# Kernel tuning notes

Hardware: AMD Instinct MI355X
Metric: run time of the kernel (lower is better)

The kernel has to match this reference:

```python
import jax, jax.numpy as jnp
import numpy as np

B, D, H, DH, NQ, NK = 64, 768, 8, 128, 256, 256


def _ln(x, g, b, eps=1e-5):
    m = x.mean(-1, keepdims=True)
    v = ((x - m) ** 2).mean(-1, keepdims=True)
    return (x - m) / jnp.sqrt(v + eps) * g + b


def setup_inputs() -> dict:
    key = jax.random.key(0)
    ks = jax.random.split(key, 16)
    w = lambda k, s: jax.random.normal(k, s, jnp.float32) * 0.02
    return {
        'emb_cause': jax.random.normal(ks[0], (B, D), jnp.float32),
        'emb_action': jax.random.normal(ks[1], (B, D), jnp.float32),
        'tok_cause': jax.random.normal(ks[2], (B, NK, D), jnp.float32),
        'tok_effect': jax.random.normal(ks[3], (B, NQ, D), jnp.float32),
        'fuse_ln_g': jnp.ones(2 * D), 'fuse_ln_b': jnp.zeros(2 * D),
        'fuse_w1': w(ks[4], (2 * D, D)), 'fuse_b1': jnp.zeros(D),
        'fuse_w2': w(ks[5], (D, D)), 'fuse_b2': jnp.zeros(D),
        'delta_ln_g': jnp.ones(D), 'delta_ln_b': jnp.zeros(D),
        'delta_w': w(ks[6], (D, D)), 'delta_b': jnp.zeros(D),
        'qg_w': w(ks[7], (D, H * DH)), 'qg_b': jnp.zeros(H * DH),
        'kg_w': w(ks[8], (D, H * DH)), 'kg_b': jnp.zeros(H * DH),
        'eff_ln_g': jnp.ones(D), 'eff_ln_b': jnp.zeros(D),
        'eff_w1': w(ks[9], (D, D)), 'eff_b1': jnp.zeros(D),
        'eff_w2': w(ks[10], (D, D)), 'eff_b2': jnp.zeros(D),
        'u_w': w(ks[11], (D, H * DH)),
        'v_w': w(ks[12], (D, H * DH)),
        'logit_scale': jnp.zeros(()),
    }


def reference(emb_cause, emb_action, tok_cause, tok_effect,
              fuse_ln_g, fuse_ln_b, fuse_w1, fuse_b1, fuse_w2, fuse_b2,
              delta_ln_g, delta_ln_b, delta_w, delta_b,
              qg_w, qg_b, kg_w, kg_b,
              eff_ln_g, eff_ln_b, eff_w1, eff_b1, eff_w2, eff_b2,
              u_w, v_w, logit_scale):
    # fuse: LN -> Linear -> GELU(exact) -> Linear (dropout = identity, eval)
    ctx_in = jnp.concatenate([emb_cause, emb_action], axis=-1)  # (B, 2D)
    h = jax.nn.gelu(_ln(ctx_in, fuse_ln_g, fuse_ln_b) @ fuse_w1 + fuse_b1, approximate=False)
    ctx = h @ fuse_w2 + fuse_b2  # (B, D)

    delta_e = _ln(ctx, delta_ln_g, delta_ln_b) @ delta_w + delta_b  # (B, D)
    pooled_effect = tok_effect.mean(axis=1)  # (B, D)
    e_shifted = pooled_effect + delta_e

    eh = jax.nn.gelu(_ln(ctx, eff_ln_g, eff_ln_b) @ eff_w1 + eff_b1, approximate=False)
    effect_pred = eh @ eff_w2 + eff_b2  # (B, D)

    q_gate = 1.0 + jnp.tanh(jax.nn.silu(ctx @ qg_w + qg_b)).reshape(B, H, DH)
    k_gate = 1.0 + jnp.tanh(jax.nn.silu(ctx @ kg_w + kg_b)).reshape(B, H, DH)

    # logit bias: torch code materializes (B,H,Nq,Nk,Dh); equivalent math is a
    # per-head inner product u.v (independent of q) broadcast over Nq.
    u = (e_shifted @ u_w).reshape(B, H, DH)            # (B, H, Dh)
    v = (tok_cause @ v_w).reshape(B, NK, H, DH)        # (B, Nk, H, Dh)
    bias = jnp.einsum('bhd,bkhd->bhk', u, v) / np.float32(np.sqrt(DH))
    logit_bias = jnp.exp(logit_scale) * jnp.broadcast_to(bias[:, :, None, :], (B, H, NQ, NK))

    return (q_gate, k_gate, e_shifted, delta_e, logit_bias, effect_pred)
```

## Files before the change

kernel.cpp:

```cpp
#include <hip/hip_runtime.h>
#include <math.h>

#define TPB 256

typedef float vf4 __attribute__((ext_vector_type(4)));

__device__ __forceinline__ float gelu_f(float x) {
    return 0.5f * x * (1.0f + erff(x * 0.70710678118654752f));
}
__device__ __forceinline__ float gate_f(float x) {
    float si = x / (1.0f + expf(-x));
    return 1.0f + tanhf(si);
}

template <class XL>
__device__ __forceinline__ void gemm_tile(XL xload, const float* __restrict__ W, int Wld, int cb,
                                          int k0, int kslice, float* part, int totN, int gcol, int s,
                                          float* __restrict__ xs, float* __restrict__ wt)
{
    const int t = threadIdx.x;
    const int tr4 = (t >> 4) << 2;
    const int tc4 = (t & 15) << 2;
    const int a  = t >> 5, kk = t & 31;
    const int wk = t >> 6, wc = t & 63;
    float xv[8], wv[8];
#pragma unroll
    for (int j = 0; j < 8; ++j) {
        xv[j] = xload(a + 8 * j, k0 + kk);
        wv[j] = W[(size_t)(k0 + wk + 4 * j) * Wld + cb + wc];
    }
    float acc[4][4] = {{0.f,0.f,0.f,0.f},{0.f,0.f,0.f,0.f},{0.f,0.f,0.f,0.f},{0.f,0.f,0.f,0.f}};
    for (int kc = 0; kc < kslice; kc += 32) {
#pragma unroll
        for (int j = 0; j < 8; ++j) {
            xs[kk * 68 + a + 8 * j] = xv[j];
            wt[(wk + 4 * j) * 68 + wc] = wv[j];
        }
        __syncthreads();
        int kn = kc + 32;
        if (kn < kslice) {
#pragma unroll
            for (int j = 0; j < 8; ++j) {
                xv[j] = xload(a + 8 * j, k0 + kn + kk);
                wv[j] = W[(size_t)(k0 + kn + wk + 4 * j) * Wld + cb + wc];
            }
        }
#pragma unroll
        for (int k = 0; k < 32; ++k) {
            float4 xq = *(const float4*)&xs[k * 68 + tr4];
            float4 wq = *(const float4*)&wt[k * 68 + tc4];
            acc[0][0] += xq.x * wq.x; acc[0][1] += xq.x * wq.y; acc[0][2] += xq.x * wq.z; acc[0][3] += xq.x * wq.w;
            acc[1][0] += xq.y * wq.x; acc[1][1] += xq.y * wq.y; acc[1][2] += xq.y * wq.z; acc[1][3] += xq.y * wq.w;
            acc[2][0] += xq.z * wq.x; acc[2][1] += xq.z * wq.y; acc[2][2] += xq.z * wq.z; acc[2][3] += xq.z * wq.w;
            acc[3][0] += xq.w * wq.x; acc[3][1] += xq.w * wq.y; acc[3][2] += xq.w * wq.z; acc[3][3] += xq.w * wq.w;
        }
        __syncthreads();
    }
    float* pp = part + (size_t)(s * 64 + tr4) * totN + gcol + tc4;
#pragma unroll
    for (int i = 0; i < 4; ++i)
#pragma unroll
        for (int j = 0; j < 4; ++j)
            pp[i * totN + j] = acc[i][j];
}

#define GEMM_LDS __shared__ float xs[32 * 68]; __shared__ float wt[32 * 68];

__device__ __forceinline__ void pool_task(const float* __restrict__ tok_effect,
                                          float* __restrict__ pp, int m, int t)
{
    int cch = m % 3, b = (m / 3) % 64, qz = m / 192;
    int c = cch * TPB + t;
    const float* base = tok_effect + (size_t)(b * 256 + qz * 64) * 768 + c;
    float s = 0.f;
#pragma unroll 16
    for (int q = 0; q < 64; ++q) s += __builtin_nontemporal_load(base + (size_t)q * 768);
    pp[(qz * 64 + b) * 768 + c] = s;
}

__global__ __launch_bounds__(256) void k_stats(const float* __restrict__ ec, const float* __restrict__ ea,
                                               float* __restrict__ stats1)
{
    int t = threadIdx.x, r = blockIdx.x;
    __shared__ float red[4];
    float v[6]; float sum = 0.f;
#pragma unroll
    for (int j = 0; j < 6; ++j) {
        int c = t + j * TPB;
        float x = (c < 768) ? ec[r * 768 + c] : ea[r * 768 + (c - 768)];
        v[j] = x; sum += x;
    }
#pragma unroll
    for (int o_ = 32; o_ > 0; o_ >>= 1) sum += __shfl_xor(sum, o_);
    if ((t & 63) == 0) red[t >> 6] = sum;
    __syncthreads();
    sum = red[0] + red[1] + red[2] + red[3];
    float mean = sum * (1.f / 1536.f);
    __syncthreads();
    float s2 = 0.f;
#pragma unroll
    for (int j = 0; j < 6; ++j) { float d = v[j] - mean; s2 += d * d; }
#pragma unroll
    for (int o_ = 32; o_ > 0; o_ >>= 1) s2 += __shfl_xor(s2, o_);
    if ((t & 63) == 0) red[t >> 6] = s2;
    __syncthreads();
    s2 = red[0] + red[1] + red[2] + red[3];
    if (t == 0) {
        stats1[2 * r]     = mean;
        stats1[2 * r + 1] = rsqrtf(s2 * (1.f / 1536.f) + 1e-5f);
    }
}

struct G1Args {
    const float *ec, *ea, *stats1, *flg, *flb, *w1;
    const float *tok_effect;
    float *part1, *pp;
};
__global__ __launch_bounds__(256) void k_g1(G1Args A)
{
    GEMM_LDS;
    if (blockIdx.x >= 144) {
        pool_task(A.tok_effect, A.pp, blockIdx.x - 144, threadIdx.x);
        return;
    }
    int ct = blockIdx.x % 12, s = blockIdx.x / 12;
    auto xl = [&](int r, int k) {
        float raw = (k < 768) ? A.ec[r * 768 + k] : A.ea[r * 768 + (k - 768)];
        float m = A.stats1[2 * r], rs = A.stats1[2 * r + 1];
        return (raw - m) * rs * A.flg[k] + A.flb[k];
    };
    gemm_tile(xl, A.w1, 768, ct * 64, s * 128, 128, A.part1, 768, ct * 64, s, xs, wt);
}

struct G2Args {
    const float *part1, *b1, *w2;
    const float *tok_effect;
    float *part2, *pp;
};
__global__ __launch_bounds__(256) void k_g2(G2Args A)
{
    GEMM_LDS;
    if (blockIdx.x >= 144) {
        pool_task(A.tok_effect, A.pp, blockIdx.x - 144 + 384, threadIdx.x);
        return;
    }
    int ct = blockIdx.x % 12, s = blockIdx.x / 12;
    auto xl = [&](int r, int k) {
        float v = A.b1[k];
#pragma unroll
        for (int q = 0; q < 12; ++q) v += A.part1[(size_t)(q * 64 + r) * 768 + k];
        return gelu_f(v);
    };
    gemm_tile(xl, A.w2, 768, ct * 64, s * 64, 64, A.part2, 768, ct * 64, s, xs, wt);
}

__global__ __launch_bounds__(256) void k_ln(const float* __restrict__ part2, const float* __restrict__ b2,
                                            float* __restrict__ ctx, float* __restrict__ stats2)
{
    int r = blockIdx.x, t = threadIdx.x;
    __shared__ float red[4];
    float v[3]; float sum = 0.f;
#pragma unroll
    for (int j = 0; j < 3; ++j) {
        int c = t + j * TPB;
        float x = b2[c];
#pragma unroll
        for (int s = 0; s < 12; ++s) x += part2[(size_t)(s * 64 + r) * 768 + c];
        v[j] = x; sum += x;
        ctx[r * 768 + c] = x;
    }
#pragma unroll
    for (int o_ = 32; o_ > 0; o_ >>= 1) sum += __shfl_xor(sum, o_);
    if ((t & 63) == 0) red[t >> 6] = sum;
    __syncthreads();
    sum = red[0] + red[1] + red[2] + red[3];
    float mean = sum * (1.f / 768.f);
    __syncthreads();
    float s2 = 0.f;
#pragma unroll
    for (int j = 0; j < 3; ++j) { float d = v[j] - mean; s2 += d * d; }
#pragma unroll
    for (int o_ = 32; o_ > 0; o_ >>= 1) s2 += __shfl_xor(s2, o_);
    if ((t & 63) == 0) red[t >> 6] = s2;
    __syncthreads();
    s2 = red[0] + red[1] + red[2] + red[3];
    if (t == 0) {
        stats2[2 * r]     = mean;
        stats2[2 * r + 1] = rsqrtf(s2 * (1.f / 768.f) + 1e-5f);
    }
}

struct GAArgs {
    const float *ctx, *stats2, *dg, *db, *eg, *eb;
    const float *delta_w, *eff_w1, *qg_w, *kg_w;
    float* partA;
};
__global__ __launch_bounds__(256) void k_gA(GAArgs A)
{
    GEMM_LDS;
    int ct = blockIdx.x % 56, s = blockIdx.x / 56;
    if (ct < 12) {
        auto xl = [&](int r, int k) {
            float m = A.stats2[2 * r], rs = A.stats2[2 * r + 1];
            return (A.ctx[r * 768 + k] - m) * rs * A.dg[k] + A.db[k];
        };
        gemm_tile(xl, A.delta_w, 768, ct * 64, s * 96, 96, A.partA, 3584, ct * 64, s, xs, wt);
    } else if (ct < 24) {
        auto xl = [&](int r, int k) {
            float m = A.stats2[2 * r], rs = A.stats2[2 * r + 1];
            return (A.ctx[r * 768 + k] - m) * rs * A.eg[k] + A.eb[k];
        };
        gemm_tile(xl, A.eff_w1, 768, (ct - 12) * 64, s * 96, 96, A.partA, 3584, ct * 64, s, xs, wt);
    } else {
        auto xl = [&](int r, int k) { return A.ctx[r * 768 + k]; };
        const float* W = (ct < 40) ? A.qg_w : A.kg_w;
        int cb = (ct < 40) ? (ct - 24) * 64 : (ct - 40) * 64;
        gemm_tile(xl, W, 1024, cb, s * 96, 96, A.partA, 3584, ct * 64, s, xs, wt);
    }
}

struct MidArgs {
    const float *partA, *pp, *delta_b, *eff_b1, *qg_b, *kg_b, *eff_w2, *u_w;
    float *partB, *out_de, *out_es, *out_qg, *out_kg;
};
__global__ __launch_bounds__(256) void k_mid(MidArgs A)
{
    GEMM_LDS;
    const int t = threadIdx.x;
    if (blockIdx.x < 28) {
#pragma unroll
        for (int ii = 0; ii < 32; ++ii) {
            int idx = blockIdx.x * TPB + t + ii * 7168;
            int r = idx / 3584, c = idx - r * 3584;
            if (c >= 768 && c < 1536) continue;
            float v = 0.f;
#pragma unroll
            for (int q = 0; q < 8; ++q) v += A.partA[(size_t)(q * 64 + r) * 3584 + c];
            if (c < 768) {
                float de = v + A.delta_b[c];
                A.out_de[r * 768 + c] = de;
                float s4 = A.pp[r * 768 + c] + A.pp[(64 + r) * 768 + c]
                         + A.pp[(128 + r) * 768 + c] + A.pp[(192 + r) * 768 + c];
                A.out_es[r * 768 + c] = de + s4 * (1.f / 256.f);
            } else if (c < 2560) {
                A.out_qg[r * 1024 + (c - 1536)] = gate_f(v + A.qg_b[c - 1536]);
            } else {
                A.out_kg[r * 1024 + (c - 2560)] = gate_f(v + A.kg_b[c - 2560]);
            }
        }
    } else {
        int m = blockIdx.x - 28;
        int ct = m % 28, s = m / 28;
        if (ct < 12) {
            auto xl = [&](int r, int k) {
                float v = A.eff_b1[k];
#pragma unroll
                for (int q = 0; q < 8; ++q) v += A.partA[(size_t)(q * 64 + r) * 3584 + 768 + k];
                return gelu_f(v);
            };
            gemm_tile(xl, A.eff_w2, 768, ct * 64, s * 96, 96, A.partB, 1792, ct * 64, s, xs, wt);
        } else {
            auto xl = [&](int r, int k) {
                float v = A.delta_b[k];
#pragma unroll
                for (int q = 0; q < 8; ++q) v += A.partA[(size_t)(q * 64 + r) * 3584 + k];
                float s4 = A.pp[r * 768 + k] + A.pp[(64 + r) * 768 + k]
                         + A.pp[(128 + r) * 768 + k] + A.pp[(192 + r) * 768 + k];
                return v + s4 * (1.f / 256.f);
            };
            gemm_tile(xl, A.u_w, 1024, (ct - 12) * 64, s * 96, 96, A.partB, 1792, ct * 64, s, xs, wt);
        }
    }
}

__global__ __launch_bounds__(256) void k_tail(const float* __restrict__ partB, const float* __restrict__ eff_b2,
                                              const float* __restrict__ v_w,
                                              float* __restrict__ out_ep, float* __restrict__ wu)
{
    const int t = threadIdx.x;
    if (blockIdx.x < 6) {
#pragma unroll
        for (int ii = 0; ii < 32; ++ii) {
            int idx = blockIdx.x * TPB + t + ii * 1536;
            int r = idx / 768, c = idx - r * 768;
            float v = eff_b2[c];
#pragma unroll
            for (int q = 0; q < 8; ++q) v += partB[(size_t)(q * 64 + r) * 1792 + c];
            out_ep[r * 768 + c] = v;
        }
    } else {
        __shared__ float us[64 * 132];
        int m = blockIdx.x - 6;
        int h = m / 12, ctile = m % 12;
        for (int n = t; n < 8192; n += TPB) {
            int b = n >> 7, d = n & 127;
            float v = 0.f;
#pragma unroll
            for (int q = 0; q < 8; ++q) v += partB[(size_t)(q * 64 + b) * 1792 + 768 + h * 128 + d];
            us[b * 132 + d] = v;
        }
        __syncthreads();
        int c = ctile * 64 + (t >> 2);
        int bo = t & 3;
        const float* vr = v_w + (size_t)c * 1024 + h * 128;
        float acc[16];
#pragma unroll
        for (int i = 0; i < 16; ++i) acc[i] = 0.f;
        for (int d = 0; d < 128; d += 4) {
            float4 w4 = *(const float4*)(vr + d);
#pragma unroll
            for (int i = 0; i < 16; ++i) {
                const float* ub = &us[(4 * i + bo) * 132 + d];
                acc[i] += w4.x * ub[0] + w4.y * ub[1] + w4.z * ub[2] + w4.w * ub[3];
            }
        }
#pragma unroll
        for (int i = 0; i < 16; ++i) {
            int b = 4 * i + bo;
            wu[(b * 8 + h) * 768 + c] = acc[i];
        }
    }
}

__global__ __launch_bounds__(512) void k_biasbc(const float* __restrict__ tok_cause, const float* __restrict__ wu,
                         const float* __restrict__ ls_ptr, float* __restrict__ out_lb)
{
    int b = blockIdx.x, kt = blockIdx.y;
    __shared__ float wuh[8 * 768];
    __shared__ float bsm[8 * 32];
    for (int n = threadIdx.x; n < 6144; n += 512)
        wuh[n] = wu[b * 6144 + n];
    __syncthreads();
    const int lane = threadIdx.x & 63, w = threadIdx.x >> 6;
    vf4 wur[3][8];
#pragma unroll
    for (int j = 0; j < 3; ++j)
#pragma unroll
        for (int h = 0; h < 8; ++h)
            wur[j][h] = *(const vf4*)&wuh[h * 768 + (lane + 64 * j) * 4];
    float scale = expf(ls_ptr[0]) * 0.08838834764831845f;
#pragma unroll
    for (int rr = 0; rr < 4; ++rr) {
        int rl = w * 4 + rr;
        int row = kt * 32 + rl;
        const vf4* tr = (const vf4*)(tok_cause + ((size_t)b * 256 + row) * 768);
        vf4 t0 = __builtin_nontemporal_load(tr + lane);
        vf4 t1 = __builtin_nontemporal_load(tr + lane + 64);
        vf4 t2 = __builtin_nontemporal_load(tr + lane + 128);
        float acc[8];
#pragma unroll
        for (int h = 0; h < 8; ++h) {
            acc[h] = t0.x * wur[0][h].x + t0.y * wur[0][h].y + t0.z * wur[0][h].z + t0.w * wur[0][h].w
                   + t1.x * wur[1][h].x + t1.y * wur[1][h].y + t1.z * wur[1][h].z + t1.w * wur[1][h].w
                   + t2.x * wur[2][h].x + t2.y * wur[2][h].y + t2.z * wur[2][h].z + t2.w * wur[2][h].w;
        }
#pragma unroll
        for (int h = 0; h < 8; ++h) {
            float vv = acc[h];
#pragma unroll
            for (int o_ = 32; o_ > 0; o_ >>= 1) vv += __shfl_xor(vv, o_);
            if (lane == 0) bsm[h * 32 + rl] = vv * scale;
        }
    }
    __syncthreads();
    const vf4* bs4 = (const vf4*)bsm;
    vf4* o4 = (vf4*)out_lb;
    int v = threadIdx.x & 7, sq0 = threadIdx.x >> 3;
#pragma unroll
    for (int it = 0; it < 32; ++it) {
        int seg = sq0 + it * 64;
        int h = seg >> 8, q = seg & 255;
        vf4 val = bs4[h * 8 + v];
        __builtin_nontemporal_store(val, &o4[(((size_t)(b * 8 + h) * 256 + q) << 6) + kt * 8 + v]);
    }
}

extern "C" void kernel_launch(void* const* d_in, const int* in_sizes, int n_in,
                              void* d_out, int out_size, void* d_ws, size_t ws_size,
                              hipStream_t stream)
{
    (void)in_sizes; (void)n_in; (void)out_size; (void)ws_size;
    const float* emb_cause  = (const float*)d_in[0];
    const float* emb_action = (const float*)d_in[1];
    const float* tok_cause  = (const float*)d_in[2];
    const float* tok_effect = (const float*)d_in[3];
    const float* fuse_ln_g  = (const float*)d_in[4];
    const float* fuse_ln_b  = (const float*)d_in[5];
    const float* fuse_w1    = (const float*)d_in[6];
    const float* fuse_b1    = (const float*)d_in[7];
    const float* fuse_w2    = (const float*)d_in[8];
    const float* fuse_b2    = (const float*)d_in[9];
    const float* delta_ln_g = (const float*)d_in[10];
    const float* delta_ln_b = (const float*)d_in[11];
    const float* delta_w    = (const float*)d_in[12];
    const float* delta_b    = (const float*)d_in[13];
    const float* qg_w       = (const float*)d_in[14];
    const float* qg_b       = (const float*)d_in[15];
    const float* kg_w       = (const float*)d_in[16];
    const float* kg_b       = (const float*)d_in[17];
    const float* eff_ln_g   = (const float*)d_in[18];
    const float* eff_ln_b   = (const float*)d_in[19];
    const float* eff_w1     = (const float*)d_in[20];
    const float* eff_b1     = (const float*)d_in[21];
    const float* eff_w2     = (const float*)d_in[22];
    const float* eff_b2     = (const float*)d_in[23];
    const float* u_w        = (const float*)d_in[24];
    const float* v_w        = (const float*)d_in[25];
    const float* logit_sc   = (const float*)d_in[26];

    float* ws = (float*)d_ws;
    float* ctx    = ws + 0;
    float* pp     = ws + 49152;
    float* wu     = ws + 245760;
    float* stats1 = ws + 638976;
    float* stats2 = ws + 639104;

    float* out    = (float*)d_out;
    float* out_qg = out + 0;
    float* out_kg = out + 65536;
    float* out_es = out + 131072;
    float* out_de = out + 180224;
    float* out_lb = out + 229376;
    float* out_ep = out + 33783808;

    float* pbase = out_lb + 20000000;
    float* part1 = pbase;
    float* part2 = pbase + 589824;
    float* partA = pbase + 1179648;
    float* partB = pbase + 3014656;

    k_stats<<<64, TPB, 0, stream>>>(emb_cause, emb_action, stats1);
    {
        G1Args A; A.ec = emb_cause; A.ea = emb_action; A.stats1 = stats1;
        A.flg = fuse_ln_g; A.flb = fuse_ln_b; A.w1 = fuse_w1;
        A.tok_effect = tok_effect; A.part1 = part1; A.pp = pp;
        k_g1<<<528, TPB, 0, stream>>>(A);
    }
    {
        G2Args A; A.part1 = part1; A.b1 = fuse_b1; A.w2 = fuse_w2;
        A.tok_effect = tok_effect; A.part2 = part2; A.pp = pp;
        k_g2<<<528, TPB, 0, stream>>>(A);
    }
    k_ln<<<64, TPB, 0, stream>>>(part2, fuse_b2, ctx, stats2);
    {
        GAArgs A; A.ctx = ctx; A.stats2 = stats2;
        A.dg = delta_ln_g; A.db = delta_ln_b; A.eg = eff_ln_g; A.eb = eff_ln_b;
        A.delta_w = delta_w; A.eff_w1 = eff_w1; A.qg_w = qg_w; A.kg_w = kg_w; A.partA = partA;
        k_gA<<<448, TPB, 0, stream>>>(A);
    }
    {
        MidArgs M; M.partA = partA; M.pp = pp;
        M.delta_b = delta_b; M.eff_b1 = eff_b1; M.qg_b = qg_b; M.kg_b = kg_b;
        M.eff_w2 = eff_w2; M.u_w = u_w; M.partB = partB;
        M.out_de = out_de; M.out_es = out_es; M.out_qg = out_qg; M.out_kg = out_kg;
        k_mid<<<252, TPB, 0, stream>>>(M);
    }
    k_tail<<<102, TPB, 0, stream>>>(partB, eff_b2, v_w, out_ep, wu);
    k_biasbc<<<dim3(64, 8), 512, 0, stream>>>(tok_cause, wu, logit_sc, out_lb);
}
```

Baseline: 140.8 us.

## Fold LN stats into first GEMM and prefetch tok_cause into cache during gA

Removes the separate k_stats launch: each GEMM block of k_g1 now computes the fuse-LayerNorm mean and rstd for all 64 rows itself, using a one-pass sum/sum-of-squares, and keeps them in shared memory. It also adds 320 extra blocks to k_gA that stream all of tok_cause (48 MB) through loads whose results are discarded, to warm the cache, and switches the bias kernel's tok_cause loads from nontemporal to normal so they can hit that cache. This trades one launch and a later HBM stream for redundant stats work per block, a less stable variance formula, and extra bandwidth use inside the GEMM phase. Whether a 48 MB prefetch survives in the MI355X last-level cache until the bias kernel runs is uncertain.

Result: slower. 155.8 us (+10.7%).

```diff
diff --git a/kernel.cpp b/kernel.cpp
--- a/kernel.cpp
+++ b/kernel.cpp
@@ -78,56 +78,50 @@
     pp[(qz * 64 + b) * 768 + c] = s;
 }
 
-__global__ __launch_bounds__(256) void k_stats(const float* __restrict__ ec, const float* __restrict__ ea,
-                                               float* __restrict__ stats1)
-{
-    int t = threadIdx.x, r = blockIdx.x;
-    __shared__ float red[4];
-    float v[6]; float sum = 0.f;
-#pragma unroll
-    for (int j = 0; j < 6; ++j) {
-        int c = t + j * TPB;
-        float x = (c < 768) ? ec[r * 768 + c] : ea[r * 768 + (c - 768)];
-        v[j] = x; sum += x;
-    }
-#pragma unroll
-    for (int o_ = 32; o_ > 0; o_ >>= 1) sum += __shfl_xor(sum, o_);
-    if ((t & 63) == 0) red[t >> 6] = sum;
-    __syncthreads();
-    sum = red[0] + red[1] + red[2] + red[3];
-    float mean = sum * (1.f / 1536.f);
-    __syncthreads();
-    float s2 = 0.f;
-#pragma unroll
-    for (int j = 0; j < 6; ++j) { float d = v[j] - mean; s2 += d * d; }
-#pragma unroll
-    for (int o_ = 32; o_ > 0; o_ >>= 1) s2 += __shfl_xor(s2, o_);
-    if ((t & 63) == 0) red[t >> 6] = s2;
-    __syncthreads();
-    s2 = red[0] + red[1] + red[2] + red[3];
-    if (t == 0) {
-        stats1[2 * r]     = mean;
-        stats1[2 * r + 1] = rsqrtf(s2 * (1.f / 1536.f) + 1e-5f);
-    }
-}
-
 struct G1Args {
-    const float *ec, *ea, *stats1, *flg, *flb, *w1;
+    const float *ec, *ea, *flg, *flb, *w1;
     const float *tok_effect;
     float *part1, *pp;
 };
 __global__ __launch_bounds__(256) void k_g1(G1Args A)
 {
     GEMM_LDS;
+    __shared__ float sred[8][64];
+    __shared__ float sst[128];
+    const int t = threadIdx.x;
     if (blockIdx.x >= 144) {
-        pool_task(A.tok_effect, A.pp, blockIdx.x - 144, threadIdx.x);
+        pool_task(A.tok_effect, A.pp, blockIdx.x - 144, t);
         return;
+    }
+    {
+        int row = t & 63, part = t >> 6;
+        const float* src = (part < 2) ? (A.ec + row * 768 + part * 384)
+                                      : (A.ea + row * 768 + (part - 2) * 384);
+        const vf4* s4 = (const vf4*)src;
+        float sum = 0.f, sq = 0.f;
+#pragma unroll 8
+        for (int j = 0; j < 96; ++j) {
+            vf4 v = s4[j];
+            sum += v.x + v.y + v.z + v.w;
+            sq  += v.x * v.x + v.y * v.y + v.z * v.z + v.w * v.w;
+        }
+        sred[part][row] = sum;
+        sred[4 + part][row] = sq;
+        __syncthreads();
+        if (t < 64) {
+            float s = sred[0][t] + sred[1][t] + sred[2][t] + sred[3][t];
+            float q = sred[4][t] + sred[5][t] + sred[6][t] + sred[7][t];
+            float mean = s * (1.f / 1536.f);
+            float var = q * (1.f / 1536.f) - mean * mean;
+            sst[2 * t]     = mean;
+            sst[2 * t + 1] = rsqrtf(var + 1e-5f);
+        }
+        __syncthreads();
     }
     int ct = blockIdx.x % 12, s = blockIdx.x / 12;
     auto xl = [&](int r, int k) {
         float raw = (k < 768) ? A.ec[r * 768 + k] : A.ea[r * 768 + (k - 768)];
-        float m = A.stats1[2 * r], rs = A.stats1[2 * r + 1];
-        return (raw - m) * rs * A.flg[k] + A.flb[k];
+        return (raw - sst[2 * r]) * sst[2 * r + 1] * A.flg[k] + A.flb[k];
     };
     gemm_tile(xl, A.w1, 768, ct * 64, s * 128, 128, A.part1, 768, ct * 64, s, xs, wt);
 }
@@ -193,11 +187,21 @@
 struct GAArgs {
     const float *ctx, *stats2, *dg, *db, *eg, *eb;
     const float *delta_w, *eff_w1, *qg_w, *kg_w;
+    const float *tok_cause;
     float* partA;
 };
 __global__ __launch_bounds__(256) void k_gA(GAArgs A)
 {
     GEMM_LDS;
+    if (blockIdx.x >= 448) {
+        const vf4* tc = (const vf4*)A.tok_cause;
+        unsigned idx = (blockIdx.x - 448) * TPB + threadIdx.x;
+        for (unsigned i = idx; i < 3145728u; i += 320u * TPB) {
+            vf4 v = tc[i];
+            asm volatile("" :: "v"(v));
+        }
+        return;
+    }
     int ct = blockIdx.x % 56, s = blockIdx.x / 56;
     if (ct < 12) {
         auto xl = [&](int r, int k) {
@@ -344,9 +348,9 @@
         int rl = w * 4 + rr;
         int row = kt * 32 + rl;
         const vf4* tr = (const vf4*)(tok_cause + ((size_t)b * 256 + row) * 768);
-        vf4 t0 = __builtin_nontemporal_load(tr + lane);
-        vf4 t1 = __builtin_nontemporal_load(tr + lane + 64);
-        vf4 t2 = __builtin_nontemporal_load(tr + lane + 128);
+        vf4 t0 = tr[lane];
+        vf4 t1 = tr[lane + 64];
+        vf4 t2 = tr[lane + 128];
         float acc[8];
 #pragma unroll
         for (int h = 0; h < 8; ++h) {
@@ -412,8 +416,7 @@
     float* ctx    = ws + 0;
     float* pp     = ws + 49152;
     float* wu     = ws + 245760;
-    float* stats1 = ws + 638976;
-    float* stats2 = ws + 639104;
+    float* stats2 = ws + 638976;
 
     float* out    = (float*)d_out;
     float* out_qg = out + 0;
@@ -429,9 +432,8 @@
     float* partA = pbase + 1179648;
     float* partB = pbase + 3014656;
 
-    k_stats<<<64, TPB, 0, stream>>>(emb_cause, emb_action, stats1);
     {
-        G1Args A; A.ec = emb_cause; A.ea = emb_action; A.stats1 = stats1;
+        G1Args A; A.ec = emb_cause; A.ea = emb_action;
         A.flg = fuse_ln_g; A.flb = fuse_ln_b; A.w1 = fuse_w1;
         A.tok_effect = tok_effect; A.part1 = part1; A.pp = pp;
         k_g1<<<528, TPB, 0, stream>>>(A);
@@ -445,8 +447,9 @@
     {
         GAArgs A; A.ctx = ctx; A.stats2 = stats2;
         A.dg = delta_ln_g; A.db = delta_ln_b; A.eg = eff_ln_g; A.eb = eff_ln_b;
-        A.delta_w = delta_w; A.eff_w1 = eff_w1; A.qg_w = qg_w; A.kg_w = kg_w; A.partA = partA;
-        k_gA<<<448, TPB, 0, stream>>>(A);
+        A.delta_w = delta_w; A.eff_w1 = eff_w1; A.qg_w = qg_w; A.kg_w = kg_w;
+        A.tok_cause = tok_cause; A.partA = partA;
+        k_gA<<<768, TPB, 0, stream>>>(A);
     }
     {
         MidArgs M; M.partA = partA; M.pp = pp;
```
